# Kernel tuning notes

Measured on AMD Instinct MI355X. Metric: run time of the kernel, lower is better.

Reference implementation:

```python
import jax, jax.numpy as jnp
import numpy as np

NUM_EXPERTS = 16
HIDDEN_DIM = 1024
TOP_K = 4
INPUT_DIM = 4096
OUTPUT_DIM = 4096
BATCH = 4096


def setup_inputs() -> dict:
    key = jax.random.key(0)
    ks = jax.random.split(key, 6)
    total_cols = NUM_EXPERTS * HIDDEN_DIM
    return {
        "x": jax.random.normal(ks[0], (BATCH, INPUT_DIM), dtype=jnp.float32),
        "gate_w": jax.random.normal(ks[1], (INPUT_DIM, NUM_EXPERTS), dtype=jnp.float32) * 0.02,
        "gate_b": jnp.zeros((NUM_EXPERTS,), dtype=jnp.float32),
        "weight": jax.random.normal(ks[2], (INPUT_DIM, total_cols), dtype=jnp.float32) * 0.01,
        "agg_w": jax.random.normal(ks[3], (total_cols, OUTPUT_DIM), dtype=jnp.float32) * 0.02,
        "agg_b": jnp.zeros((OUTPUT_DIM,), dtype=jnp.float32),
    }


def reference(x, gate_w, gate_b, weight, agg_w, agg_b):
    # 1) gating logits (batch, E), 2) sum over batch -> (E,)
    gating_logits = x @ gate_w + gate_b
    gating_sum = gating_logits.sum(axis=0)
    # 3) global top-k expert selection -> binary mask over experts
    _, topk_inds = jax.lax.top_k(gating_sum, TOP_K)
    expert_mask = jnp.zeros((NUM_EXPERTS,), dtype=x.dtype).at[topk_inds].set(1.0)
    # 4/5) block-sparse matmul: mask replicated over all row blocks, so each
    # expert's column block [e*H:(e+1)*H] is x @ W_block if selected else 0.
    out_sparse = x @ weight  # (batch, E*H)
    col_mask = jnp.repeat(expert_mask, HIDDEN_DIM)  # (E*H,)
    out_sparse = out_sparse * col_mask[None, :]
    # 6) aggregator
    final_out = out_sparse @ agg_w + agg_b
    return final_out
```

## Files before the change

### kernel.cpp

```cpp
#include <hip/hip_runtime.h>
#include <hip/hip_bf16.h>


#define BATCH 4096
#define DIN 4096
#define NE 16
#define HD 1024
#define TOPK 4
#define TOTC (NE * HD)
#define NT 64

using bf16 = __hip_bfloat16;
typedef __attribute__((ext_vector_type(8))) short short8;
typedef __attribute__((ext_vector_type(4))) float f32x4;

__device__ inline short f2bs(float f) {
  __hip_bfloat16 h = __float2bfloat16(f);
  return *reinterpret_cast<short*>(&h);
}

__global__ void k_cvtsum(const float* __restrict__ x, bf16* __restrict__ xb,
                         float* __restrict__ colsum) {
  const int t = threadIdx.x;
  const int lane = t & 63;
  const int w = t >> 6;
  const int c = blockIdx.x * 256 + lane * 4;
  const int r0 = blockIdx.y * 128 + w * 32;
  float4 s = {0.f, 0.f, 0.f, 0.f};
  for (int i = 0; i < 32; ++i) {
    size_t off = (size_t)(r0 + i) * DIN + c;
    float4 v = *reinterpret_cast<const float4*>(x + off);
    s.x += v.x; s.y += v.y; s.z += v.z; s.w += v.w;
    ushort4 b;
    b.x = (unsigned short)f2bs(v.x); b.y = (unsigned short)f2bs(v.y);
    b.z = (unsigned short)f2bs(v.z); b.w = (unsigned short)f2bs(v.w);
    *reinterpret_cast<ushort4*>(reinterpret_cast<char*>(xb) + off * 2) = b;
  }
  __shared__ float sm[4][256];
  sm[w][lane * 4 + 0] = s.x; sm[w][lane * 4 + 1] = s.y;
  sm[w][lane * 4 + 2] = s.z; sm[w][lane * 4 + 3] = s.w;
  __syncthreads();
  float tot = sm[0][t] + sm[1][t] + sm[2][t] + sm[3][t];
  atomicAdd(&colsum[blockIdx.x * 256 + t], tot);
}

__global__ void k_gate(const float* __restrict__ colsum, const float* __restrict__ gw,
                       const float* __restrict__ gb, int* __restrict__ ids) {
  __shared__ float red[4][16];
  __shared__ float gs[16];
  int t = threadIdx.x;
  int e = t & 15, kg = t >> 4;
  float p = 0.f;
  for (int k = kg; k < DIN; k += 16) p += colsum[k] * gw[(size_t)k * NE + e];
  p += __shfl_down(p, 32);
  p += __shfl_down(p, 16);
  if ((t & 63) < 16) red[t >> 6][e] = p;
  __syncthreads();
  if (t < 16) gs[t] = red[0][t] + red[1][t] + red[2][t] + red[3][t] + (float)BATCH * gb[t];
  __syncthreads();
  if (t == 0) {
    float v[16];
    #pragma unroll
    for (int i = 0; i < 16; ++i) v[i] = gs[i];
    for (int j = 0; j < TOPK; ++j) {
      int bi = 0;
      float bv = v[0];
      for (int i2 = 1; i2 < 16; ++i2)
        if (v[i2] > bv) { bv = v[i2]; bi = i2; }
      ids[j] = bi;
      v[bi] = -3.4e38f;
    }
  }
}

__global__ void k_gather(const float* __restrict__ w, const float* __restrict__ a,
                         const int* __restrict__ ids,
                         bf16* __restrict__ wbt, bf16* __restrict__ abt) {
  __shared__ float tile[64 * 65];
  const int t = threadIdx.x;
  const int tc = t & 15, kr = t >> 4;
  const int tk = t & 7, nr0 = t >> 3;
  for (int tl = blockIdx.x; tl < 8192; tl += 2048) {
    const int wsel = tl < 4096;
    const int tidx = wsel ? tl : tl - 4096;
    const int k0 = (tidx & 63) * 64, n0 = (tidx >> 6) * 64;
    if (wsel) {
      const int e = ids[n0 >> 10];
      const int wc0 = e * HD + (n0 & 1023);
      #pragma unroll
      for (int j = 0; j < 4; ++j) {
        int kk = kr + j * 16;
        float4 v = *reinterpret_cast<const float4*>(w + (size_t)(k0 + kk) * TOTC + wc0 + tc * 4);
        float* dst = &tile[kk * 65 + tc * 4];
        dst[0] = v.x; dst[1] = v.y; dst[2] = v.z; dst[3] = v.w;
      }
    } else {
      const int e = ids[k0 >> 10];
      const int ar0 = e * HD + (k0 & 1023);
      #pragma unroll
      for (int j = 0; j < 4; ++j) {
        int kk = kr + j * 16;
        float4 v = *reinterpret_cast<const float4*>(a + (size_t)(ar0 + kk) * 4096 + n0 + tc * 4);
        float* dst = &tile[kk * 65 + tc * 4];
        dst[0] = v.x; dst[1] = v.y; dst[2] = v.z; dst[3] = v.w;
      }
    }
    __syncthreads();
    bf16* dstp = wsel ? wbt : abt;
    #pragma unroll
    for (int i = 0; i < 2; ++i) {
      int n = n0 + nr0 + i * 32;
      short8 r;
      #pragma unroll
      for (int m = 0; m < 8; ++m) r[m] = f2bs(tile[(tk * 8 + m) * 65 + nr0 + i * 32]);
      *reinterpret_cast<short8*>(dstp + (size_t)n * DIN + k0 + tk * 8) = r;
    }
    __syncthreads();
  }
}

#define MFMA_BF16 __builtin_amdgcn_mfma_f32_16x16x32_bf16
#define VM4 asm volatile("s_waitcnt vmcnt(4)" ::: "memory")
#define VM0 asm volatile("s_waitcnt vmcnt(0)" ::: "memory")
#define NOST ((void)0)

#define PHA(BUF, STG, GATE)                                                     \
  do {                                                                          \
    _Pragma("unroll") for (int nf = 0; nf < 4; ++nf) {                          \
      bfrag[nf][0] = LDB(BUF, nf, 0);                                           \
      bfrag[nf][1] = LDB(BUF, nf, 1);                                           \
    }                                                                           \
    short8 af[4][2];                                                            \
    _Pragma("unroll") for (int m = 0; m < 4; ++m) {                             \
      af[m][0] = LDA(BUF, m, 0);                                                \
      af[m][1] = LDA(BUF, m, 1);                                                \
    }                                                                           \
    STG;                                                                        \
    GATE;                                                                       \
    __builtin_amdgcn_s_barrier();                                               \
    _Pragma("unroll") for (int kk = 0; kk < 2; ++kk)                            \
      _Pragma("unroll") for (int m = 0; m < 4; ++m)                             \
        _Pragma("unroll") for (int nf = 0; nf < 4; ++nf)                        \
          acc[m][nf] = MFMA_BF16(af[m][kk], bfrag[nf][kk], acc[m][nf], 0, 0, 0); \
  } while (0)

#define PHB(BUF, STG, GATE)                                                     \
  do {                                                                          \
    short8 af[4][2];                                                            \
    _Pragma("unroll") for (int m = 0; m < 4; ++m) {                             \
      af[m][0] = LDA(BUF, m + 4, 0);                                            \
      af[m][1] = LDA(BUF, m + 4, 1);                                            \
    }                                                                           \
    STG;                                                                        \
    GATE;                                                                       \
    __builtin_amdgcn_s_barrier();                                               \
    _Pragma("unroll") for (int kk = 0; kk < 2; ++kk)                            \
      _Pragma("unroll") for (int m = 0; m < 4; ++m)                             \
        _Pragma("unroll") for (int nf = 0; nf < 4; ++nf)                        \
          acc[m + 4][nf] = MFMA_BF16(af[m][kk], bfrag[nf][kk], acc[m + 4][nf], 0, 0, 0); \
  } while (0)

template <int STORE_F32>
__global__ __launch_bounds__(512, 2) void k_gemm8(
    const bf16* __restrict__ A, const bf16* __restrict__ Bt,
    bf16* __restrict__ Cb, float* __restrict__ Cf, const float* __restrict__ bias) {
  __shared__ __align__(16) char smraw[131072];
  const int t = threadIdx.x;
  const int lane = t & 63;
  const int w = t >> 6;
  const int wr = w >> 2;
  const int wc = w & 3;

  const int bid = blockIdx.x;
  const int xcd = bid & 7;
  const int i = bid >> 3;
  const int bm = ((xcd >> 1) * 4 + (i & 3)) * 256;
  const int bn = ((xcd & 1) * 8 + (i >> 2)) * 256;

  f32x4 acc[8][4] = {};
  short8 bfrag[4][2];

  const int srow = w * 16 + (lane >> 3);
  const int sgr = lane & 7;

  auto STAGE_A = [&](int buf, int kt) {
    #pragma unroll
    for (int half = 0; half < 2; ++half) {
      char* lb = smraw + buf * 65536 + half * 16384 + w * 2048 + lane * 16;
      #pragma unroll
      for (int i2 = 0; i2 < 2; ++i2) {
        int r = srow + i2 * 8;
        const bf16* g = A + (size_t)(bm + half * 128 + r) * 4096 + kt * 64 + ((sgr ^ (r & 7)) * 8);
        __builtin_amdgcn_global_load_lds(
            (const __attribute__((address_space(1))) void*)g,
            (__attribute__((address_space(3))) void*)(lb + i2 * 1024), 16, 0, 0);
      }
    }
  };
  auto STAGE_B = [&](int buf, int kt) {
    #pragma unroll
    for (int half = 0; half < 2; ++half) {
      char* lb = smraw + buf * 65536 + 32768 + half * 16384 + w * 2048 + lane * 16;
      #pragma unroll
      for (int i2 = 0; i2 < 2; ++i2) {
        int r = srow + i2 * 8;
        const bf16* g = Bt + (size_t)(bn + half * 128 + r) * 4096 + kt * 64 + ((sgr ^ (r & 7)) * 8);
        __builtin_amdgcn_global_load_lds(
            (const __attribute__((address_space(1))) void*)g,
            (__attribute__((address_space(3))) void*)(lb + i2 * 1024), 16, 0, 0);
      }
    }
  };
  auto LDA = [&](int buf, int mf, int kk) -> short8 {
    int r = mf * 16 + (lane & 15);
    int kb = ((kk * 4 + (lane >> 4)) ^ (r & 7)) * 16;
    return *reinterpret_cast<const short8*>(smraw + buf * 65536 + wr * 16384 + r * 128 + kb);
  };
  auto LDB = [&](int buf, int nf, int kk) -> short8 {
    int nc = wc * 64 + nf * 16 + (lane & 15);
    int half = nc >> 7, r = nc & 127;
    int kb = ((kk * 4 + (lane >> 4)) ^ (r & 7)) * 16;
    return *reinterpret_cast<const short8*>(smraw + buf * 65536 + 32768 + half * 16384 + r * 128 + kb);
  };

  STAGE_B(0, 0);
  STAGE_A(0, 0);
  STAGE_B(1, 1);
  VM4;
  __builtin_amdgcn_s_barrier();

  for (int tt = 0; tt < 31; ++tt) {
    const int a = 2 * tt;
    PHA(0, STAGE_A(1, a + 1), NOST);
    PHB(0, STAGE_B(0, a + 2), VM4);
    PHA(1, STAGE_A(0, a + 2), NOST);
    PHB(1, STAGE_B(1, a + 3), VM4);
  }
  PHA(0, STAGE_A(1, 63), NOST);
  PHB(0, NOST, VM0);
  PHA(1, NOST, NOST);
  PHB(1, NOST, NOST);

  const int cr = (lane >> 4) * 4;
  const int cc = lane & 15;
  #pragma unroll
  for (int mf = 0; mf < 8; ++mf) {
    #pragma unroll
    for (int nf = 0; nf < 4; ++nf) {
      int row = bm + wr * 128 + mf * 16 + cr;
      int col = bn + wc * 64 + nf * 16 + cc;
      #pragma unroll
      for (int r = 0; r < 4; ++r) {
        if constexpr (STORE_F32) {
          Cf[(size_t)(row + r) * 4096 + col] = acc[mf][nf][r] + bias[col];
        } else {
          Cb[(size_t)(row + r) * 4096 + col] = __float2bfloat16(acc[mf][nf][r]);
        }
      }
    }
  }
}

extern "C" void kernel_launch(void* const* d_in, const int* in_sizes, int n_in,
                              void* d_out, int out_size, void* d_ws, size_t ws_size,
                              hipStream_t stream) {
  const float* x = (const float*)d_in[0];
  const float* gate_w = (const float*)d_in[1];
  const float* gate_b = (const float*)d_in[2];
  const float* weight = (const float*)d_in[3];
  const float* agg_w = (const float*)d_in[4];
  const float* agg_b = (const float*)d_in[5];
  float* out = (float*)d_out;
  char* ws = (char*)d_ws;

  float* colsum = (float*)ws;
  int* ids = (int*)(ws + 16384);
  bf16* mid = (bf16*)(ws + (4u << 20));
  bf16* abt = (bf16*)(ws + (36u << 20));
  bf16* xb = (bf16*)d_out;
  bf16* wbt = (bf16*)((char*)d_out + (32u << 20));

  hipMemsetAsync(colsum, 0, DIN * sizeof(float), stream);
  k_cvtsum<<<dim3(16, 32), 256, 0, stream>>>(x, xb, colsum);
  k_gate<<<1, 256, 0, stream>>>(colsum, gate_w, gate_b, ids);
  k_gather<<<2048, 256, 0, stream>>>(weight, agg_w, ids, wbt, abt);
  k_gemm8<0><<<256, 512, 0, stream>>>(xb, wbt, mid, nullptr, nullptr);
  k_gemm8<1><<<256, 512, 0, stream>>>(mid, abt, nullptr, out, agg_b);
}
```

Measured before the change: 373.8 us.

## Double-buffer gather tile and stage bf16 GEMM epilogue through LDS for wide stores

The gather kernel now alternates between two shared tiles, which lets it drop the trailing barrier of each iteration. The bf16 output path of the GEMM writes each wave's 16x64 accumulator patch to LDS and reads it back row-wise. It then emits two 16-byte bf16 stores per lane instead of scattered 2-byte stores. This costs extra LDS traffic and a barrier, and it relies on the double buffer alone being enough for gather correctness across iterations.

```diff
diff --git a/kernel.cpp b/kernel.cpp
--- a/kernel.cpp
+++ b/kernel.cpp
@@ -76,14 +76,16 @@
 __global__ void k_gather(const float* __restrict__ w, const float* __restrict__ a,
                          const int* __restrict__ ids,
                          bf16* __restrict__ wbt, bf16* __restrict__ abt) {
-  __shared__ float tile[64 * 65];
+  __shared__ float tile[2][64 * 65];
   const int t = threadIdx.x;
   const int tc = t & 15, kr = t >> 4;
   const int tk = t & 7, nr0 = t >> 3;
-  for (int tl = blockIdx.x; tl < 8192; tl += 2048) {
+  int pb = 0;
+  for (int tl = blockIdx.x; tl < 8192; tl += 2048, pb ^= 1) {
     const int wsel = tl < 4096;
     const int tidx = wsel ? tl : tl - 4096;
     const int k0 = (tidx & 63) * 64, n0 = (tidx >> 6) * 64;
+    float* tb = tile[pb];
     if (wsel) {
       const int e = ids[n0 >> 10];
       const int wc0 = e * HD + (n0 & 1023);
@@ -91,7 +93,7 @@
       for (int j = 0; j < 4; ++j) {
         int kk = kr + j * 16;
         float4 v = *reinterpret_cast<const float4*>(w + (size_t)(k0 + kk) * TOTC + wc0 + tc * 4);
-        float* dst = &tile[kk * 65 + tc * 4];
+        float* dst = &tb[kk * 65 + tc * 4];
         dst[0] = v.x; dst[1] = v.y; dst[2] = v.z; dst[3] = v.w;
       }
     } else {
@@ -101,7 +103,7 @@
       for (int j = 0; j < 4; ++j) {
         int kk = kr + j * 16;
         float4 v = *reinterpret_cast<const float4*>(a + (size_t)(ar0 + kk) * 4096 + n0 + tc * 4);
-        float* dst = &tile[kk * 65 + tc * 4];
+        float* dst = &tb[kk * 65 + tc * 4];
         dst[0] = v.x; dst[1] = v.y; dst[2] = v.z; dst[3] = v.w;
       }
     }
@@ -112,10 +114,9 @@
       int n = n0 + nr0 + i * 32;
       short8 r;
       #pragma unroll
-      for (int m = 0; m < 8; ++m) r[m] = f2bs(tile[(tk * 8 + m) * 65 + nr0 + i * 32]);
+      for (int m = 0; m < 8; ++m) r[m] = f2bs(tb[(tk * 8 + m) * 65 + nr0 + i * 32]);
       *reinterpret_cast<short8*>(dstp + (size_t)n * DIN + k0 + tk * 8) = r;
     }
-    __syncthreads();
   }
 }
 
@@ -243,20 +244,46 @@
 
   const int cr = (lane >> 4) * 4;
   const int cc = lane & 15;
-  #pragma unroll
-  for (int mf = 0; mf < 8; ++mf) {
-    #pragma unroll
-    for (int nf = 0; nf < 4; ++nf) {
-      int row = bm + wr * 128 + mf * 16 + cr;
-      int col = bn + wc * 64 + nf * 16 + cc;
-      #pragma unroll
-      for (int r = 0; r < 4; ++r) {
-        if constexpr (STORE_F32) {
+  if constexpr (STORE_F32) {
+    #pragma unroll
+    for (int mf = 0; mf < 8; ++mf) {
+      #pragma unroll
+      for (int nf = 0; nf < 4; ++nf) {
+        int row = bm + wr * 128 + mf * 16 + cr;
+        int col = bn + wc * 64 + nf * 16 + cc;
+        #pragma unroll
+        for (int r = 0; r < 4; ++r)
           Cf[(size_t)(row + r) * 4096 + col] = acc[mf][nf][r] + bias[col];
-        } else {
-          Cb[(size_t)(row + r) * 4096 + col] = __float2bfloat16(acc[mf][nf][r]);
-        }
-      }
+      }
+    }
+  } else {
+    __builtin_amdgcn_s_barrier();
+    char* patch = smraw + w * 4352;
+    const int r16 = lane >> 2;
+    const int cg = (lane & 3) * 16;
+    #pragma unroll
+    for (int mf = 0; mf < 8; ++mf) {
+      #pragma unroll
+      for (int nf = 0; nf < 4; ++nf)
+        #pragma unroll
+        for (int r = 0; r < 4; ++r)
+          *reinterpret_cast<float*>(patch + (cr + r) * 272 + (nf * 16 + cc) * 4) = acc[mf][nf][r];
+      asm volatile("s_waitcnt lgkmcnt(0)" ::: "memory");
+      const char* rp = patch + r16 * 272 + cg * 4;
+      float4 v0 = *reinterpret_cast<const float4*>(rp);
+      float4 v1 = *reinterpret_cast<const float4*>(rp + 16);
+      float4 v2 = *reinterpret_cast<const float4*>(rp + 32);
+      float4 v3 = *reinterpret_cast<const float4*>(rp + 48);
+      asm volatile("s_waitcnt lgkmcnt(0)" ::: "memory");
+      short8 p0, p1;
+      p0[0] = f2bs(v0.x); p0[1] = f2bs(v0.y); p0[2] = f2bs(v0.z); p0[3] = f2bs(v0.w);
+      p0[4] = f2bs(v1.x); p0[5] = f2bs(v1.y); p0[6] = f2bs(v1.z); p0[7] = f2bs(v1.w);
+      p1[0] = f2bs(v2.x); p1[1] = f2bs(v2.y); p1[2] = f2bs(v2.z); p1[3] = f2bs(v2.w);
+      p1[4] = f2bs(v3.x); p1[5] = f2bs(v3.y); p1[6] = f2bs(v3.z); p1[7] = f2bs(v3.w);
+      int row = bm + wr * 128 + mf * 16 + r16;
+      bf16* dst = Cb + (size_t)row * 4096 + bn + wc * 64 + cg;
+      *reinterpret_cast<short8*>(dst) = p0;
+      *reinterpret_cast<short8*>(dst + 8) = p1;
     }
   }
 }
```

New measurement: 377.2 us. About the same (+0.9%).
